# Performance work log

Measured on AMD Instinct MI355X. Metric: run time of the kernel, lower is better.

The kernel has to match this reference:

```python
import jax, jax.numpy as jnp
import numpy as np

EPS = 1e-5
INF = 1e5


def setup_inputs() -> dict:
    key = jax.random.key(0)
    ks = iter(jax.random.split(key, 32))
    B, N, F, H, NH, C = 2, 384, 64, 64, 4, 32
    def lin(k, fi, fo):
        return jax.random.normal(k, (fi, fo), jnp.float32) / np.sqrt(fi).astype(np.float32)
    d = {}
    d['h'] = jax.random.normal(next(ks), (B, N, F), jnp.float32)
    d['x'] = jax.random.normal(next(ks), (B, N, 3), jnp.float32)
    # edge_model (ConcatenationFilter): Linear(2F+1,H), SiLU, Linear(H,H), SiLU
    d['We0'] = lin(next(ks), 2 * F + 1, H); d['be0'] = jnp.zeros(H, jnp.float32)
    d['We1'] = lin(next(ks), H, H);         d['be1'] = jnp.zeros(H, jnp.float32)
    # semantic_attention_mlp: Linear(H, n_heads), LeakyReLU(0.2)
    d['Ws'] = lin(next(ks), H, NH);         d['bs'] = jnp.zeros(NH, jnp.float32)
    # coefficients_mlp: Linear(H,H), SiLU, Linear(H,C)
    d['Wc0'] = lin(next(ks), H, H);         d['bc0'] = jnp.zeros(H, jnp.float32)
    d['Wc1'] = lin(next(ks), H, C);         d['bc1'] = jnp.zeros(C, jnp.float32)
    # post_norm_mlp: Linear(C,H), SiLU, Linear(H,H)
    d['Wp0'] = lin(next(ks), C, H);         d['bp0'] = jnp.zeros(H, jnp.float32)
    d['Wp1'] = lin(next(ks), H, H);         d['bp1'] = jnp.zeros(H, jnp.float32)
    # coordinate_mlp: Linear(H,H), SiLU, Linear(H,1,bias=False) init gain 1e-3
    d['Wx0'] = lin(next(ks), H, H);         d['bx0'] = jnp.zeros(H, jnp.float32)
    d['Wx1'] = lin(next(ks), H, 1) * 1e-3
    # node_mlp: Linear(NH*H + H + F, H), SiLU, Linear(H, F)
    d['Wn0'] = lin(next(ks), NH * H + H + F, H); d['bn0'] = jnp.zeros(H, jnp.float32)
    d['Wn1'] = lin(next(ks), H, F);         d['bn1'] = jnp.zeros(F, jnp.float32)
    d['log_gamma'] = jnp.zeros(NH, jnp.float32)
    return d


def _forward(h, x, We0, be0, We1, be1, Ws, bs, Wc0, bc0, Wc1, bc1,
             Wp0, bp0, Wp1, bp1, Wx0, bx0, Wx1, Wn0, bn0, Wn1, bn1, log_gamma):
    B, N, F = h.shape
    silu = jax.nn.silu

    # pairwise displacements and distances: (B,N,N,3), (B,N,N,1)
    x_minus_xt = x[:, :, None, :] - x[:, None, :, :]
    norm = jnp.sqrt(jnp.sum(x_minus_xt * x_minus_xt, axis=-1, keepdims=True) + EPS)

    # pairwise node-feature concat + distance -> edge MLP (ConcatenationFilter)
    hi = jnp.broadcast_to(h[:, :, None, :], (B, N, N, F))
    hj = jnp.broadcast_to(h[:, None, :, :], (B, N, N, F))
    e_in = jnp.concatenate([hi, hj, norm], axis=-1)           # (B,N,N,2F+1)
    h_e = silu(silu(e_in @ We0 + be0) @ We1 + be1)            # (B,N,N,H)

    eye = jnp.eye(N, dtype=h.dtype)[None, :, :, None]         # mask self-edges

    # euclidean attention per head, softmax over neighbors j (axis=-2)
    eu = jax.nn.softmax(-(norm + INF * eye) * jnp.exp(log_gamma), axis=-2)  # (B,N,N,NH)
    # semantic attention
    sem_logits = jax.nn.leaky_relu(h_e @ Ws + bs, 0.2) - INF * eye
    sem = jax.nn.softmax(sem_logits, axis=-2)                 # (B,N,N,NH)
    comb = eu * sem
    comb = comb / (jnp.sum(comb, axis=-2, keepdims=True) + EPS)

    # attention-weighted multi-head edge features, aggregated over neighbors
    h_e_att = (comb[..., :, None] * h_e[..., None, :]).reshape(B, N, N, -1)  # (B,N,N,NH*H)
    h_e_agg = jnp.sum(h_e_att, axis=-2)                       # (B,N,NH*H)

    # spatial attention: equivariant combinations of unit direction vectors
    coeff = silu(h_e @ Wc0 + bc0) @ Wc1 + bc1                 # (B,N,N,C)
    x_hat = x_minus_xt / (norm + EPS)                         # (B,N,N,3)
    combinations = coeff[..., :, None] * x_hat[..., None, :]  # (B,N,N,C,3)
    comb_sum = jnp.mean(combinations, axis=2)                 # mean over j -> (B,N,C,3)
    comb_norm = jnp.sum(comb_sum * comb_sum, axis=-1)         # (B,N,C)
    h_comb = silu(comb_norm @ Wp0 + bp0) @ Wp1 + bp1          # (B,N,H)

    # node update (residual)
    node_in = jnp.concatenate([h, h_e_agg, h_comb], axis=-1)
    h_out = h + (silu(node_in @ Wn0 + bn0) @ Wn1 + bn1)

    # coordinate update: scalar-gated displacements, mean over neighbors
    scale = silu(h_e @ Wx0 + bx0) @ Wx1                       # (B,N,N,1)
    x_out = x + jnp.mean(x_minus_xt * scale, axis=2)          # (B,N,3)
    return h_out, x_out


def reference(h, x, We0, be0, We1, be1, Ws, bs, Wc0, bc0, Wc1, bc1,
              Wp0, bp0, Wp1, bp1, Wx0, bx0, Wx1, Wn0, bn0, Wn1, bn1, log_gamma):
    return _forward(h, x, We0, be0, We1, be1, Ws, bs, Wc0, bc0, Wc1, bc1,
                    Wp0, bp0, Wp1, bp1, Wx0, bx0, Wx1, Wn0, bn0, Wn1, bn1, log_gamma)
```

## Files before the change

### kernel.cpp

```cpp
#include <hip/hip_runtime.h>

#define NPT 384
#define NB 2
#define NROW (NB*NPT)
#define NT 6
#define HOFF 49152
#define RECB 1024
#define REC_OFF 424960

typedef unsigned short u16;
typedef unsigned int u32;
typedef __bf16 bf16x8 __attribute__((ext_vector_type(8)));
typedef float f32x4 __attribute__((ext_vector_type(4)));

struct alignas(16) U4 { u32 x, y, z, w; };

constexpr float kEPS = 1e-5f;
constexpr float kINF = 1e5f;

__device__ __forceinline__ u16 f2b(float f) { __bf16 b = (__bf16)f; return __builtin_bit_cast(u16, b); }
__device__ __forceinline__ u32 pk2(float lo, float hi) { return (u32)f2b(lo) | ((u32)f2b(hi) << 16); }
__device__ __forceinline__ float b2f(u32 u) { return __uint_as_float(u << 16); }
__device__ __forceinline__ float silu_f(float v) { return v * __builtin_amdgcn_rcpf(1.f + __expf(-v)); }
__device__ __forceinline__ float wredmax(float v) {
#pragma unroll
  for (int m = 32; m >= 1; m >>= 1) v = fmaxf(v, __shfl_xor(v, m, 64));
  return v;
}
__device__ __forceinline__ float wredsum(float v) {
#pragma unroll
  for (int m = 32; m >= 1; m >>= 1) v += __shfl_xor(v, m, 64);
  return v;
}
__device__ __forceinline__ void up8(U4 u, float* f) {
  f[0] = b2f(u.x & 0xffffu); f[1] = b2f(u.x >> 16);
  f[2] = b2f(u.y & 0xffffu); f[3] = b2f(u.y >> 16);
  f[4] = b2f(u.z & 0xffffu); f[5] = b2f(u.z >> 16);
  f[6] = b2f(u.w & 0xffffu); f[7] = b2f(u.w >> 16);
}

__global__ __launch_bounds__(64) void sake_prep(
    const float* __restrict__ h, const float* __restrict__ We0,
    const float* __restrict__ be0, const float* __restrict__ We1,
    const float* __restrict__ Wc0, const float* __restrict__ Wc1,
    const float* __restrict__ Wx0, const float* __restrict__ Ws,
    float* __restrict__ U, float* __restrict__ V, u16* __restrict__ WT)
{
  const int t = threadIdx.x;
  const int blk = blockIdx.x;
  if (blk < NROW) {
    __shared__ float hs[64];
    hs[t] = h[blk * 64 + t];
    __syncthreads();
    float u = be0[t], v = 0.f;
#pragma unroll 8
    for (int k = 0; k < 64; k++) {
      float hv = hs[k];
      u = fmaf(hv, We0[k * 64 + t], u);
      v = fmaf(hv, We0[(64 + k) * 64 + t], v);
    }
    U[blk * 64 + t] = u;
    V[blk * 64 + t] = v;
  } else {
    const int wsel = blk - NROW;
    if (wsel == 4) {
      u16* dst = WT + 14336;
      for (int o = t; o < 16 * 64; o += 64) {
        int c = o >> 6, k = o & 63;
        dst[o] = (c < 4) ? f2b(Ws[k * 4 + c]) : (u16)0;
      }
      return;
    }
    const float* src; int nout; u16* dst;
    if      (wsel == 0) { src = We1; nout = 64; dst = WT;         }
    else if (wsel == 1) { src = Wc0; nout = 64; dst = WT + 4096;  }
    else if (wsel == 2) { src = Wx0; nout = 64; dst = WT + 8192;  }
    else                { src = Wc1; nout = 32; dst = WT + 12288; }
    const int total = 64 * nout;
    for (int o = t; o < total; o += 64) {
      int n = o >> 6, k = o & 63;
      dst[o] = f2b(src[k * nout + n]);
    }
  }
}

struct MainArgs {
  const float *x, *U, *V;
  const u16 *We1T, *Wc0T, *Wx0T, *Wc1T, *WsPT;
  const float *We0, *bs, *be1, *bc0, *bc1, *bx0, *Wx1, *log_gamma;
  char* rec;
};

template<bool DUALT>
__device__ __forceinline__ void gemm64(const u16* aT, const u16* __restrict__ wG,
                                       const float* bias, u16* oT, u16* oTT, int w, int lane)
{
  const int m0 = w << 4;
  const int arow = m0 + (lane & 15);
  const int r7 = arow & 7;
  const int kg = lane >> 4;
  bf16x8 a0 = *(const bf16x8*)(aT + arow * 64 + ((kg ^ r7) << 3));
  bf16x8 a1 = *(const bf16x8*)(aT + arow * 64 + ((((kg + 4)) ^ r7) << 3));
#pragma unroll
  for (int nt = 0; nt < 4; nt++) {
    const int col = (nt << 4) + (lane & 15);
    const u16* wrow = wG + col * 64;
    bf16x8 b0 = *(const bf16x8*)(wrow + (kg << 3));
    bf16x8 b1 = *(const bf16x8*)(wrow + 32 + (kg << 3));
    f32x4 acc = {0.f, 0.f, 0.f, 0.f};
    acc = __builtin_amdgcn_mfma_f32_16x16x32_bf16(a0, b0, acc, 0, 0, 0);
    acc = __builtin_amdgcn_mfma_f32_16x16x32_bf16(a1, b1, acc, 0, 0, 0);
    const float bv = bias[col];
    const int cs = col >> 3, ce = col & 7;
#pragma unroll
    for (int r = 0; r < 4; r++) {
      const int row = m0 + (kg << 2) + r;
      const u16 v = f2b(silu_f(acc[r] + bv));
      oT[row * 64 + ((cs ^ (row & 7)) << 3) + ce] = v;
      if constexpr (DUALT)
        oTT[col * 64 + ((((row >> 3)) ^ (col & 7)) << 3) + (row & 7)] = v;
    }
  }
}

__global__ __launch_bounds__(256, 5) void sake_main(MainArgs A)
{
  __shared__ __align__(16) u16 buf0[64 * 64];
  __shared__ __align__(16) u16 hes[64 * 64];
  __shared__ __align__(16) u16 hesT[64 * 64];
  __shared__ __align__(16) u16 reg3[64 * 32];
  __shared__ float raw_lds[64 * 5];
  __shared__ float disp[64][3];
  __shared__ float nrm_s[64];
  __shared__ float sU[64], wd[64], sbe1[64], sbc0[64], sbx0[64], sWx1[64];
  __shared__ float sbc1[32], sbs[4], sgam[4];

  const int t = threadIdx.x;
  const int w = t >> 6, lane = t & 63;
  const int bt = blockIdx.x;
  const int i = bt % NPT;
  const int bj = bt / NPT;
  const int jt = bj % NT, b = bj / NT;
  const int bi = b * NPT + i;
  const int j0 = jt << 6;
  const int jj2 = t >> 2, q4 = t & 3;
  char* rec = A.rec + (size_t)(bi * NT + jt) * RECB;

  const int j = j0 + jj2;
  const float* xp = &A.x[(b * NPT + j) * 3];
  const float xj0 = xp[0], xj1 = xp[1], xj2 = xp[2];
  const float xi0 = A.x[bi * 3 + 0], xi1 = A.x[bi * 3 + 1], xi2 = A.x[bi * 3 + 2];
  const float4* vp = (const float4*)(A.V + (size_t)(b * NPT + j) * 64 + q4 * 16);
  const float4 v0_ = vp[0], v1_ = vp[1], v2_ = vp[2], v3_ = vp[3];

  if (t < 64) {
    sU[t]   = A.U[bi * 64 + t];
    wd[t]   = A.We0[128 * 64 + t];
    sbe1[t] = A.be1[t];
    sbc0[t] = A.bc0[t];
    sbx0[t] = A.bx0[t];
    sWx1[t] = A.Wx1[t];
    if (t < 32) sbc1[t] = A.bc1[t];
    if (t < 4) { sbs[t] = A.bs[t]; sgam[t] = __expf(A.log_gamma[t]); }
  }
  __syncthreads();

  float cA0 = 0, cA1 = 0, cA2 = 0, xA0 = 0, xA1 = 0, xA2 = 0;

  {
    float dx0 = xi0 - xj0, dx1 = xi1 - xj1, dx2 = xi2 - xj2;
    float nr = sqrtf(fmaf(dx0, dx0, fmaf(dx1, dx1, fmaf(dx2, dx2, kEPS))));
    if (q4 == 0) { disp[jj2][0] = dx0; disp[jj2][1] = dx1; disp[jj2][2] = dx2; nrm_s[jj2] = nr; }
    float vv[16] = {v0_.x, v0_.y, v0_.z, v0_.w, v1_.x, v1_.y, v1_.z, v1_.w,
                    v2_.x, v2_.y, v2_.z, v2_.w, v3_.x, v3_.y, v3_.z, v3_.w};
    float sv[16];
#pragma unroll
    for (int e = 0; e < 16; e++) {
      const int f = q4 * 16 + e;
      sv[e] = silu_f(sU[f] + vv[e] + nr * wd[f]);
    }
    U4 lo, hi;
    lo.x = pk2(sv[0], sv[1]);   lo.y = pk2(sv[2], sv[3]);
    lo.z = pk2(sv[4], sv[5]);   lo.w = pk2(sv[6], sv[7]);
    hi.x = pk2(sv[8], sv[9]);   hi.y = pk2(sv[10], sv[11]);
    hi.z = pk2(sv[12], sv[13]); hi.w = pk2(sv[14], sv[15]);
    const int r7 = jj2 & 7;
    *(U4*)(buf0 + jj2 * 64 + (((q4 * 2) ^ r7) << 3)) = lo;
    *(U4*)(buf0 + jj2 * 64 + (((q4 * 2 + 1) ^ r7) << 3)) = hi;
  }
  gemm64<true>(buf0, A.We1T, sbe1, hes, hesT, w, lane);
  gemm64<false>(hes, A.Wc0T, sbc0, buf0, nullptr, w, lane);
  {
    const int m0 = w << 4;
    const int arow = m0 + (lane & 15);
    const int r7a = arow & 7;
    const int kg = lane >> 4;
    bf16x8 a0 = *(const bf16x8*)(buf0 + arow * 64 + ((kg ^ r7a) << 3));
    bf16x8 a1 = *(const bf16x8*)(buf0 + arow * 64 + (((kg + 4) ^ r7a) << 3));
#pragma unroll
    for (int nt = 0; nt < 2; nt++) {
      const int col = (nt << 4) + (lane & 15);
      const u16* wrow = A.Wc1T + col * 64;
      bf16x8 b0 = *(const bf16x8*)(wrow + (kg << 3));
      bf16x8 b1 = *(const bf16x8*)(wrow + 32 + (kg << 3));
      f32x4 acc = {0.f, 0.f, 0.f, 0.f};
      acc = __builtin_amdgcn_mfma_f32_16x16x32_bf16(a0, b0, acc, 0, 0, 0);
      acc = __builtin_amdgcn_mfma_f32_16x16x32_bf16(a1, b1, acc, 0, 0, 0);
      const float bv = sbc1[col];
#pragma unroll
      for (int r = 0; r < 4; r++) {
        const int row = m0 + (kg << 2) + r;
        reg3[row * 32 + col] = f2b(acc[r] + bv);
      }
    }
  }
  {
    const int c = t & 31, g = t >> 5;
#pragma unroll
    for (int it = 0; it < 8; ++it) {
      const int jj = (g << 3) + it;
      const float s = b2f(reg3[jj * 32 + c]) * __builtin_amdgcn_rcpf(nrm_s[jj] + kEPS);
      cA0 = fmaf(s, disp[jj][0], cA0);
      cA1 = fmaf(s, disp[jj][1], cA1);
      cA2 = fmaf(s, disp[jj][2], cA2);
    }
  }
  gemm64<false>(hes, A.Wx0T, sbx0, buf0, nullptr, w, lane);
  {
    const int jj = jj2;
    const int r7 = jj & 7;
    float acc = 0.f;
#pragma unroll
    for (int c2 = 0; c2 < 2; c2++) {
      const int c = q4 * 2 + c2;
      U4 u = *(const U4*)(buf0 + jj * 64 + ((c ^ r7) << 3));
      float f8[8]; up8(u, f8);
#pragma unroll
      for (int e = 0; e < 8; e++) acc = fmaf(f8[e], sWx1[c * 8 + e], acc);
    }
    acc += __shfl_xor(acc, 1, 64);
    acc += __shfl_xor(acc, 2, 64);
    if (q4 == 0) {
      xA0 = fmaf(disp[jj][0], acc, xA0);
      xA1 = fmaf(disp[jj][1], acc, xA1);
      xA2 = fmaf(disp[jj][2], acc, xA2);
    }
  }
  {
    const int m0 = w << 4;
    const int arow = m0 + (lane & 15);
    const int r7a = arow & 7;
    const int kg = lane >> 4;
    bf16x8 a0 = *(const bf16x8*)(hes + arow * 64 + ((kg ^ r7a) << 3));
    bf16x8 a1 = *(const bf16x8*)(hes + arow * 64 + (((kg + 4) ^ r7a) << 3));
    const u16* wrow = A.WsPT + (lane & 15) * 64;
    bf16x8 b0 = *(const bf16x8*)(wrow + (kg << 3));
    bf16x8 b1 = *(const bf16x8*)(wrow + 32 + (kg << 3));
    f32x4 acc = {0.f, 0.f, 0.f, 0.f};
    acc = __builtin_amdgcn_mfma_f32_16x16x32_bf16(a0, b0, acc, 0, 0, 0);
    acc = __builtin_amdgcn_mfma_f32_16x16x32_bf16(a1, b1, acc, 0, 0, 0);
    if ((lane & 15) < 4) {
#pragma unroll
      for (int r = 0; r < 4; r++)
        raw_lds[(m0 + (kg << 2) + r) * 5 + (lane & 15)] = acc[r];
    }
  }
  __syncthreads();

  float* cascr = (float*)hes;
  cascr[t * 3 + 0] = cA0; cascr[t * 3 + 1] = cA1; cascr[t * 3 + 2] = cA2;
  if (q4 == 0) {
    float* xs = (float*)hes + 768;
    xs[jj2 * 3 + 0] = xA0; xs[jj2 * 3 + 1] = xA1; xs[jj2 * 3 + 2] = xA2;
  }
  {
    const int jj = lane, head = w;
    float raw = raw_lds[jj * 5 + head] + sbs[head];
    float bsem = (raw > 0.f) ? raw : 0.2f * raw;
    const bool self = (j0 + jj) == i;
    if (self) bsem -= kINF;
    const float aeu = -(nrm_s[jj] + (self ? kINF : 0.f)) * sgam[head];
    const float L = aeu + bsem;
    const float mL = wredmax(L);
    const float eL = __expf(L - mL);
    const float SL = wredsum(eL);
    const float mb = wredmax(bsem);
    const float Sb = wredsum(__expf(bsem - mb));
    const float Sa = wredsum(__expf(aeu));
    u16* E = reg3 + 1024;
    E[head * 64 + (((jj >> 3) ^ head) << 3) + (jj & 7)] = f2b(eL);
    if (lane == 0) {
      float* sp = (float*)(rec + 908) + head * 5;
      sp[0] = mL; sp[1] = SL; sp[2] = mb; sp[3] = Sb; sp[4] = Sa;
    }
  }
  __syncthreads();

  {
    const int kg = lane >> 4;
    const int erow = lane & 15;
    const int e7 = erow & 7;
    const u16* E = reg3 + 1024;
    bf16x8 ea0 = *(const bf16x8*)(E + erow * 64 + ((kg ^ e7) << 3));
    bf16x8 ea1 = *(const bf16x8*)(E + erow * 64 + (((kg + 4) ^ e7) << 3));
    const int f = (w << 4) + (lane & 15);
    const int f7 = f & 7;
    bf16x8 hb0 = *(const bf16x8*)(hesT + f * 64 + ((kg ^ f7) << 3));
    bf16x8 hb1 = *(const bf16x8*)(hesT + f * 64 + (((kg + 4) ^ f7) << 3));
    f32x4 aF = {0.f, 0.f, 0.f, 0.f};
    aF = __builtin_amdgcn_mfma_f32_16x16x32_bf16(ea0, hb0, aF, 0, 0, 0);
    aF = __builtin_amdgcn_mfma_f32_16x16x32_bf16(ea1, hb1, aF, 0, 0, 0);
    if (kg == 0) {
      u16* rA = (u16*)rec;
#pragma unroll
      for (int r = 0; r < 4; r++) rA[r * 64 + (w << 4) + (lane & 15)] = f2b(aF[r]);
    }
  }
  if (t < 96) {
    const int c = t & 31, d = t >> 5;
    float s = 0.f;
#pragma unroll
    for (int g = 0; g < 8; g++) s += cascr[(g * 32 + c) * 3 + d];
    ((float*)(rec + 512))[d * 32 + c] = s;
  } else if (t < 99) {
    const int d = t - 96;
    float s = 0.f;
    for (int k = 0; k < 64; k++) s += ((float*)hes + 768)[k * 3 + d];
    ((float*)(rec + 896))[d] = s;
  }
}

struct MergeArgs {
  const float *h, *x, *Wp0, *bp0, *Wp1, *bp1, *Wn0, *bn0, *Wn1, *bn1;
  const char* rec;
  float* out;
};

__global__ __launch_bounds__(256) void sake_merge(MergeArgs M)
{
  __shared__ float sc[NT][20];
  __shared__ float wAl[NT][4];
  __shared__ float coefh[4];
  __shared__ float node_in[384];
  __shared__ float cmv[96];
  __shared__ float nrm32[32];
  __shared__ float t0s[64];
  __shared__ float scr[256];

  const int t = threadIdx.x;
  const int bi = blockIdx.x;
  const char* rb = M.rec + (size_t)bi * NT * RECB;

  if (t < NT * 20) {
    const int tt = t / 20, k = t % 20;
    sc[tt][k] = ((const float*)(rb + tt * RECB + 908))[k];
  }
  if (t < 64) node_in[t] = M.h[bi * 64 + t];
  __syncthreads();
  if (t < 4) {
    const int hh = t;
    float mL = -1e30f, mb = -1e30f;
    for (int tt = 0; tt < NT; tt++) {
      mL = fmaxf(mL, sc[tt][hh * 5 + 0]);
      mb = fmaxf(mb, sc[tt][hh * 5 + 2]);
    }
    float SL = 0.f, Sb = 0.f, Sa = 0.f;
    for (int tt = 0; tt < NT; tt++) {
      const float wa = __expf(sc[tt][hh * 5 + 0] - mL);
      wAl[tt][hh] = wa;
      SL = fmaf(wa, sc[tt][hh * 5 + 1], SL);
      Sb = fmaf(__expf(sc[tt][hh * 5 + 2] - mb), sc[tt][hh * 5 + 3], Sb);
      Sa += sc[tt][hh * 5 + 4];
    }
    const float Ff = __expf(mL - mb);
    coefh[hh] = Ff / fmaf(SL, Ff, kEPS * Sa * Sb);
  }
  __syncthreads();
  {
    const int hh = t >> 6, f = t & 63;
    float s = 0.f;
#pragma unroll
    for (int tt = 0; tt < NT; tt++)
      s = fmaf(wAl[tt][hh], b2f(((const u16*)(rb + tt * RECB))[hh * 64 + f]), s);
    node_in[64 + hh * 64 + f] = s * coefh[hh];
  }
  if (t < 96) {
    float s = 0.f;
#pragma unroll
    for (int tt = 0; tt < NT; tt++) s += ((const float*)(rb + tt * RECB + 512))[t];
    cmv[t] = s * (1.f / 384.f);
  }
  if (t >= 128 && t < 131) {
    const int d = t - 128;
    float s = 0.f;
#pragma unroll
    for (int tt = 0; tt < NT; tt++) s += ((const float*)(rb + tt * RECB + 896))[d];
    M.out[HOFF + bi * 3 + d] = M.x[bi * 3 + d] + s * (1.f / 384.f);
  }
  __syncthreads();
  if (t < 32) {
    const float v0 = cmv[t], v1 = cmv[32 + t], v2 = cmv[64 + t];
    nrm32[t] = v0 * v0 + v1 * v1 + v2 * v2;
  }
  __syncthreads();
  if (t < 64) {
    float a = M.bp0[t];
    for (int c = 0; c < 32; c++) a = fmaf(nrm32[c], M.Wp0[c * 64 + t], a);
    t0s[t] = silu_f(a);
  }
  __syncthreads();
  if (t < 64) {
    float a = M.bp1[t];
    for (int k = 0; k < 64; k++) a = fmaf(t0s[k], M.Wp1[k * 64 + t], a);
    node_in[320 + t] = a;
  }
  __syncthreads();
  {
    const int f = t & 63, q = t >> 6;
    float a = 0.f;
    const int k0 = q * 96;
    for (int k = 0; k < 96; k++) a = fmaf(node_in[k0 + k], M.Wn0[(k0 + k) * 64 + f], a);
    scr[t] = a;
  }
  __syncthreads();
  if (t < 64) {
    const float s = scr[t] + scr[64 + t] + scr[128 + t] + scr[192 + t] + M.bn0[t];
    t0s[t] = silu_f(s);
  }
  __syncthreads();
  if (t < 64) {
    float a = M.bn1[t];
    for (int k = 0; k < 64; k++) a = fmaf(t0s[k], M.Wn1[k * 64 + t], a);
    M.out[bi * 64 + t] = M.h[bi * 64 + t] + a;
  }
}

extern "C" void kernel_launch(void* const* d_in, const int* in_sizes, int n_in,
                              void* d_out, int out_size, void* d_ws, size_t ws_size,
                              hipStream_t stream)
{
  (void)in_sizes; (void)n_in; (void)out_size; (void)ws_size;
  const float* h   = (const float*)d_in[0];
  const float* x   = (const float*)d_in[1];
  const float* We0 = (const float*)d_in[2];
  const float* be0 = (const float*)d_in[3];
  const float* We1 = (const float*)d_in[4];
  const float* be1 = (const float*)d_in[5];
  const float* Ws  = (const float*)d_in[6];
  const float* bs  = (const float*)d_in[7];
  const float* Wc0 = (const float*)d_in[8];
  const float* bc0 = (const float*)d_in[9];
  const float* Wc1 = (const float*)d_in[10];
  const float* bc1 = (const float*)d_in[11];
  const float* Wp0 = (const float*)d_in[12];
  const float* bp0 = (const float*)d_in[13];
  const float* Wp1 = (const float*)d_in[14];
  const float* bp1 = (const float*)d_in[15];
  const float* Wx0 = (const float*)d_in[16];
  const float* bx0 = (const float*)d_in[17];
  const float* Wx1 = (const float*)d_in[18];
  const float* Wn0 = (const float*)d_in[19];
  const float* bn0 = (const float*)d_in[20];
  const float* Wn1 = (const float*)d_in[21];
  const float* bn1 = (const float*)d_in[22];
  const float* lg  = (const float*)d_in[23];

  float* U = (float*)d_ws;
  float* V = U + NROW * 64;
  u16* WT = (u16*)(V + NROW * 64);
  char* rec = (char*)d_ws + REC_OFF;

  sake_prep<<<NROW + 5, 64, 0, stream>>>(h, We0, be0, We1, Wc0, Wc1, Wx0, Ws, U, V, WT);

  MainArgs A;
  A.x = x; A.U = U; A.V = V;
  A.We1T = WT; A.Wc0T = WT + 4096; A.Wx0T = WT + 8192; A.Wc1T = WT + 12288;
  A.WsPT = WT + 14336;
  A.We0 = We0; A.bs = bs; A.be1 = be1; A.bc0 = bc0; A.bc1 = bc1;
  A.bx0 = bx0; A.Wx1 = Wx1; A.log_gamma = lg;
  A.rec = rec;
  sake_main<<<NROW * NT, 256, 0, stream>>>(A);

  MergeArgs Mg;
  Mg.h = h; Mg.x = x;
  Mg.Wp0 = Wp0; Mg.bp0 = bp0; Mg.Wp1 = Wp1; Mg.bp1 = bp1;
  Mg.Wn0 = Wn0; Mg.bn0 = bn0; Mg.Wn1 = Wn1; Mg.bn1 = bn1;
  Mg.rec = rec; Mg.out = (float*)d_out;
  sake_merge<<<NROW, 256, 0, stream>>>(Mg);
}
```

Measured before the change: 98.15 us.

## Transpose MFMA operand roles so activations stay in registers across chained GEMMs

Swaps the GEMM operand roles so weights are the A operand and the per-edge activations the B operand. Each wave's activation fragment is read from LDS once and reused across the consecutive small GEMMs, with packed 8-byte output stores. The shared-memory staging of biases and small vectors is replaced by direct global float4 loads, which removes one block barrier. Launch bounds drop from 5 to 4 blocks per CU, giving more registers but less occupancy.

```diff
diff --git a/kernel.cpp b/kernel.cpp
--- a/kernel.cpp
+++ b/kernel.cpp
@@ -14,6 +14,7 @@
 typedef float f32x4 __attribute__((ext_vector_type(4)));
 
 struct alignas(16) U4 { u32 x, y, z, w; };
+struct alignas(8)  U2 { u32 x, y; };
 
 constexpr float kEPS = 1e-5f;
 constexpr float kINF = 1e5f;
@@ -91,49 +92,63 @@
   char* rec;
 };
 
-template<bool DUALT>
-__device__ __forceinline__ void gemm64(const u16* aT, const u16* __restrict__ wG,
-                                       const float* bias, u16* oT, u16* oTT, int w, int lane)
+__device__ __forceinline__ void readB(const u16* tile, int j, int kg, bf16x8& f0, bf16x8& f1) {
+  const int r7 = j & 7;
+  f0 = *(const bf16x8*)(tile + j * 64 + ((kg ^ r7) << 3));
+  f1 = *(const bf16x8*)(tile + j * 64 + (((kg + 4) ^ r7) << 3));
+}
+
+template<int NNT, bool SILU_, int NCH, bool DUALT>
+__device__ __forceinline__ void gemmT(const u16* __restrict__ wG, const float* __restrict__ biasG,
+                                      bf16x8 bf0, bf16x8 bf1, u16* out, u16* oTT, int w, int lane)
 {
-  const int m0 = w << 4;
-  const int arow = m0 + (lane & 15);
-  const int r7 = arow & 7;
+  const int j = (w << 4) + (lane & 15);
   const int kg = lane >> 4;
-  bf16x8 a0 = *(const bf16x8*)(aT + arow * 64 + ((kg ^ r7) << 3));
-  bf16x8 a1 = *(const bf16x8*)(aT + arow * 64 + ((((kg + 4)) ^ r7) << 3));
-#pragma unroll
-  for (int nt = 0; nt < 4; nt++) {
-    const int col = (nt << 4) + (lane & 15);
-    const u16* wrow = wG + col * 64;
-    bf16x8 b0 = *(const bf16x8*)(wrow + (kg << 3));
-    bf16x8 b1 = *(const bf16x8*)(wrow + 32 + (kg << 3));
+  const int jm = j & (NCH - 1);
+#pragma unroll
+  for (int nt = 0; nt < NNT; nt++) {
+    const int nrow = (nt << 4) + (lane & 15);
+    bf16x8 a0 = *(const bf16x8*)(wG + nrow * 64 + (kg << 3));
+    bf16x8 a1 = *(const bf16x8*)(wG + nrow * 64 + 32 + (kg << 3));
     f32x4 acc = {0.f, 0.f, 0.f, 0.f};
-    acc = __builtin_amdgcn_mfma_f32_16x16x32_bf16(a0, b0, acc, 0, 0, 0);
-    acc = __builtin_amdgcn_mfma_f32_16x16x32_bf16(a1, b1, acc, 0, 0, 0);
-    const float bv = bias[col];
-    const int cs = col >> 3, ce = col & 7;
-#pragma unroll
-    for (int r = 0; r < 4; r++) {
-      const int row = m0 + (kg << 2) + r;
-      const u16 v = f2b(silu_f(acc[r] + bv));
-      oT[row * 64 + ((cs ^ (row & 7)) << 3) + ce] = v;
-      if constexpr (DUALT)
-        oTT[col * 64 + ((((row >> 3)) ^ (col & 7)) << 3) + (row & 7)] = v;
-    }
-  }
-}
-
-__global__ __launch_bounds__(256, 5) void sake_main(MainArgs A)
+    acc = __builtin_amdgcn_mfma_f32_16x16x32_bf16(a0, bf0, acc, 0, 0, 0);
+    acc = __builtin_amdgcn_mfma_f32_16x16x32_bf16(a1, bf1, acc, 0, 0, 0);
+    const int n0 = (nt << 4) + (kg << 2);
+    const float4 bv = *(const float4*)(biasG + n0);
+    float s0, s1, s2, s3;
+    if constexpr (SILU_) {
+      s0 = silu_f(acc[0] + bv.x); s1 = silu_f(acc[1] + bv.y);
+      s2 = silu_f(acc[2] + bv.z); s3 = silu_f(acc[3] + bv.w);
+    } else {
+      s0 = acc[0] + bv.x; s1 = acc[1] + bv.y;
+      s2 = acc[2] + bv.z; s3 = acc[3] + bv.w;
+    }
+    const u16 q0 = f2b(s0), q1 = f2b(s1), q2 = f2b(s2), q3 = f2b(s3);
+    U2 pkd; pkd.x = (u32)q0 | ((u32)q1 << 16); pkd.y = (u32)q2 | ((u32)q3 << 16);
+    const int c = n0 >> 3;
+    *(U2*)(out + j * (NCH * 8) + (((c ^ jm) << 3) + (n0 & 7))) = pkd;
+    if constexpr (DUALT) {
+      const int jq = (j >> 3), j7 = j & 7;
+      const u16 qs[4] = {q0, q1, q2, q3};
+#pragma unroll
+      for (int r = 0; r < 4; r++) {
+        const int f = n0 + r;
+        oTT[f * 64 + ((jq ^ (f & 7)) << 3) + j7] = qs[r];
+      }
+    }
+  }
+}
+
+__global__ __launch_bounds__(256, 4) void sake_main(MainArgs A)
 {
   __shared__ __align__(16) u16 buf0[64 * 64];
   __shared__ __align__(16) u16 hes[64 * 64];
   __shared__ __align__(16) u16 hesT[64 * 64];
-  __shared__ __align__(16) u16 reg3[64 * 32];
+  __shared__ __align__(16) u16 coeff[64 * 32];
+  __shared__ __align__(16) u16 E_lds[16 * 64];
   __shared__ float raw_lds[64 * 5];
   __shared__ float disp[64][3];
   __shared__ float nrm_s[64];
-  __shared__ float sU[64], wd[64], sbe1[64], sbc0[64], sbx0[64], sWx1[64];
-  __shared__ float sbc1[32], sbs[4], sgam[4];
 
   const int t = threadIdx.x;
   const int w = t >> 6, lane = t & 63;
@@ -146,26 +161,16 @@
   const int jj2 = t >> 2, q4 = t & 3;
   char* rec = A.rec + (size_t)(bi * NT + jt) * RECB;
 
-  const int j = j0 + jj2;
-  const float* xp = &A.x[(b * NPT + j) * 3];
+  const int jrow = j0 + jj2;
+  const float* xp = &A.x[(b * NPT + jrow) * 3];
   const float xj0 = xp[0], xj1 = xp[1], xj2 = xp[2];
   const float xi0 = A.x[bi * 3 + 0], xi1 = A.x[bi * 3 + 1], xi2 = A.x[bi * 3 + 2];
-  const float4* vp = (const float4*)(A.V + (size_t)(b * NPT + j) * 64 + q4 * 16);
+  const float4* vp = (const float4*)(A.V + (size_t)(b * NPT + jrow) * 64 + q4 * 16);
   const float4 v0_ = vp[0], v1_ = vp[1], v2_ = vp[2], v3_ = vp[3];
-
-  if (t < 64) {
-    sU[t]   = A.U[bi * 64 + t];
-    wd[t]   = A.We0[128 * 64 + t];
-    sbe1[t] = A.be1[t];
-    sbc0[t] = A.bc0[t];
-    sbx0[t] = A.bx0[t];
-    sWx1[t] = A.Wx1[t];
-    if (t < 32) sbc1[t] = A.bc1[t];
-    if (t < 4) { sbs[t] = A.bs[t]; sgam[t] = __expf(A.log_gamma[t]); }
-  }
-  __syncthreads();
-
-  float cA0 = 0, cA1 = 0, cA2 = 0, xA0 = 0, xA1 = 0, xA2 = 0;
+  const float4* Up = (const float4*)(A.U + bi * 64 + q4 * 16);
+  const float4 u0_ = Up[0], u1_ = Up[1], u2_ = Up[2], u3_ = Up[3];
+  const float4* Wd = (const float4*)(A.We0 + 128 * 64 + q4 * 16);
+  const float4 w0_ = Wd[0], w1_ = Wd[1], w2_ = Wd[2], w3_ = Wd[3];
 
   {
     float dx0 = xi0 - xj0, dx1 = xi1 - xj1, dx2 = xi2 - xj2;
@@ -173,12 +178,13 @@
     if (q4 == 0) { disp[jj2][0] = dx0; disp[jj2][1] = dx1; disp[jj2][2] = dx2; nrm_s[jj2] = nr; }
     float vv[16] = {v0_.x, v0_.y, v0_.z, v0_.w, v1_.x, v1_.y, v1_.z, v1_.w,
                     v2_.x, v2_.y, v2_.z, v2_.w, v3_.x, v3_.y, v3_.z, v3_.w};
+    float uu[16] = {u0_.x, u0_.y, u0_.z, u0_.w, u1_.x, u1_.y, u1_.z, u1_.w,
+                    u2_.x, u2_.y, u2_.z, u2_.w, u3_.x, u3_.y, u3_.z, u3_.w};
+    float ww[16] = {w0_.x, w0_.y, w0_.z, w0_.w, w1_.x, w1_.y, w1_.z, w1_.w,
+                    w2_.x, w2_.y, w2_.z, w2_.w, w3_.x, w3_.y, w3_.z, w3_.w};
     float sv[16];
 #pragma unroll
-    for (int e = 0; e < 16; e++) {
-      const int f = q4 * 16 + e;
-      sv[e] = silu_f(sU[f] + vv[e] + nr * wd[f]);
-    }
+    for (int e = 0; e < 16; e++) sv[e] = silu_f(uu[e] + vv[e] + nr * ww[e]);
     U4 lo, hi;
     lo.x = pk2(sv[0], sv[1]);   lo.y = pk2(sv[2], sv[3]);
     lo.z = pk2(sv[4], sv[5]);   lo.w = pk2(sv[6], sv[7]);
@@ -188,44 +194,39 @@
     *(U4*)(buf0 + jj2 * 64 + (((q4 * 2) ^ r7) << 3)) = lo;
     *(U4*)(buf0 + jj2 * 64 + (((q4 * 2 + 1) ^ r7) << 3)) = hi;
   }
-  gemm64<true>(buf0, A.We1T, sbe1, hes, hesT, w, lane);
-  gemm64<false>(hes, A.Wc0T, sbc0, buf0, nullptr, w, lane);
-  {
-    const int m0 = w << 4;
-    const int arow = m0 + (lane & 15);
-    const int r7a = arow & 7;
-    const int kg = lane >> 4;
-    bf16x8 a0 = *(const bf16x8*)(buf0 + arow * 64 + ((kg ^ r7a) << 3));
-    bf16x8 a1 = *(const bf16x8*)(buf0 + arow * 64 + (((kg + 4) ^ r7a) << 3));
-#pragma unroll
-    for (int nt = 0; nt < 2; nt++) {
-      const int col = (nt << 4) + (lane & 15);
-      const u16* wrow = A.Wc1T + col * 64;
-      bf16x8 b0 = *(const bf16x8*)(wrow + (kg << 3));
-      bf16x8 b1 = *(const bf16x8*)(wrow + 32 + (kg << 3));
-      f32x4 acc = {0.f, 0.f, 0.f, 0.f};
-      acc = __builtin_amdgcn_mfma_f32_16x16x32_bf16(a0, b0, acc, 0, 0, 0);
-      acc = __builtin_amdgcn_mfma_f32_16x16x32_bf16(a1, b1, acc, 0, 0, 0);
-      const float bv = sbc1[col];
-#pragma unroll
-      for (int r = 0; r < 4; r++) {
-        const int row = m0 + (kg << 2) + r;
-        reg3[row * 32 + col] = f2b(acc[r] + bv);
-      }
-    }
-  }
+
+  const int j = (w << 4) + (lane & 15);
+  const int kg = lane >> 4;
+
+  bf16x8 bh0, bh1;
+  readB(buf0, j, kg, bh0, bh1);
+  gemmT<4, true, 8, true>(A.We1T, A.be1, bh0, bh1, hes, hesT, w, lane);
+
+  bf16x8 he0, he1;
+  readB(hes, j, kg, he0, he1);
+
+  gemmT<4, true, 8, false>(A.Wc0T, A.bc0, he0, he1, buf0, nullptr, w, lane);
+  bf16x8 c10, c11;
+  readB(buf0, j, kg, c10, c11);
+  gemmT<2, false, 4, false>(A.Wc1T, A.bc1, c10, c11, coeff, nullptr, w, lane);
+
+  float cA0 = 0, cA1 = 0, cA2 = 0, xA0 = 0, xA1 = 0, xA2 = 0;
   {
     const int c = t & 31, g = t >> 5;
+    const int cc = c >> 3, ce = c & 7;
 #pragma unroll
     for (int it = 0; it < 8; ++it) {
       const int jj = (g << 3) + it;
-      const float s = b2f(reg3[jj * 32 + c]) * __builtin_amdgcn_rcpf(nrm_s[jj] + kEPS);
+      const float s = b2f(coeff[jj * 32 + ((cc ^ (jj & 3)) << 3) + ce]) *
+                      __builtin_amdgcn_rcpf(nrm_s[jj] + kEPS);
       cA0 = fmaf(s, disp[jj][0], cA0);
       cA1 = fmaf(s, disp[jj][1], cA1);
       cA2 = fmaf(s, disp[jj][2], cA2);
     }
   }
-  gemm64<false>(hes, A.Wx0T, sbx0, buf0, nullptr, w, lane);
+
+  gemmT<4, true, 8, false>(A.Wx0T, A.bx0, he0, he1, buf0, nullptr, w, lane);
+
   {
     const int jj = jj2;
     const int r7 = jj & 7;
@@ -235,8 +236,12 @@
       const int c = q4 * 2 + c2;
       U4 u = *(const U4*)(buf0 + jj * 64 + ((c ^ r7) << 3));
       float f8[8]; up8(u, f8);
-#pragma unroll
-      for (int e = 0; e < 8; e++) acc = fmaf(f8[e], sWx1[c * 8 + e], acc);
+      const float4* wx = (const float4*)(A.Wx1 + c * 8);
+      const float4 wxa = wx[0], wxb = wx[1];
+      acc = fmaf(f8[0], wxa.x, acc); acc = fmaf(f8[1], wxa.y, acc);
+      acc = fmaf(f8[2], wxa.z, acc); acc = fmaf(f8[3], wxa.w, acc);
+      acc = fmaf(f8[4], wxb.x, acc); acc = fmaf(f8[5], wxb.y, acc);
+      acc = fmaf(f8[6], wxb.z, acc); acc = fmaf(f8[7], wxb.w, acc);
     }
     acc += __shfl_xor(acc, 1, 64);
     acc += __shfl_xor(acc, 2, 64);
@@ -246,11 +251,11 @@
       xA2 = fmaf(disp[jj][2], acc, xA2);
     }
   }
+
   {
     const int m0 = w << 4;
     const int arow = m0 + (lane & 15);
     const int r7a = arow & 7;
-    const int kg = lane >> 4;
     bf16x8 a0 = *(const bf16x8*)(hes + arow * 64 + ((kg ^ r7a) << 3));
     bf16x8 a1 = *(const bf16x8*)(hes + arow * 64 + (((kg + 4) ^ r7a) << 3));
     const u16* wrow = A.WsPT + (lane & 15) * 64;
@@ -267,19 +272,19 @@
   }
   __syncthreads();
 
-  float* cascr = (float*)hes;
+  float* cascr = (float*)buf0;
+  float* xscr = (float*)buf0 + 768;
   cascr[t * 3 + 0] = cA0; cascr[t * 3 + 1] = cA1; cascr[t * 3 + 2] = cA2;
-  if (q4 == 0) {
-    float* xs = (float*)hes + 768;
-    xs[jj2 * 3 + 0] = xA0; xs[jj2 * 3 + 1] = xA1; xs[jj2 * 3 + 2] = xA2;
-  }
+  if (q4 == 0) { xscr[jj2 * 3 + 0] = xA0; xscr[jj2 * 3 + 1] = xA1; xscr[jj2 * 3 + 2] = xA2; }
+
   {
     const int jj = lane, head = w;
-    float raw = raw_lds[jj * 5 + head] + sbs[head];
+    float raw = raw_lds[jj * 5 + head] + A.bs[head];
     float bsem = (raw > 0.f) ? raw : 0.2f * raw;
     const bool self = (j0 + jj) == i;
     if (self) bsem -= kINF;
-    const float aeu = -(nrm_s[jj] + (self ? kINF : 0.f)) * sgam[head];
+    const float gam = __expf(A.log_gamma[head]);
+    const float aeu = -(nrm_s[jj] + (self ? kINF : 0.f)) * gam;
     const float L = aeu + bsem;
     const float mL = wredmax(L);
     const float eL = __expf(L - mL);
@@ -287,8 +292,7 @@
     const float mb = wredmax(bsem);
     const float Sb = wredsum(__expf(bsem - mb));
     const float Sa = wredsum(__expf(aeu));
-    u16* E = reg3 + 1024;
-    E[head * 64 + (((jj >> 3) ^ head) << 3) + (jj & 7)] = f2b(eL);
+    E_lds[head * 64 + (((jj >> 3) ^ head) << 3) + (jj & 7)] = f2b(eL);
     if (lane == 0) {
       float* sp = (float*)(rec + 908) + head * 5;
       sp[0] = mL; sp[1] = SL; sp[2] = mb; sp[3] = Sb; sp[4] = Sa;
@@ -297,12 +301,10 @@
   __syncthreads();
 
   {
-    const int kg = lane >> 4;
     const int erow = lane & 15;
     const int e7 = erow & 7;
-    const u16* E = reg3 + 1024;
-    bf16x8 ea0 = *(const bf16x8*)(E + erow * 64 + ((kg ^ e7) << 3));
-    bf16x8 ea1 = *(const bf16x8*)(E + erow * 64 + (((kg + 4) ^ e7) << 3));
+    bf16x8 ea0 = *(const bf16x8*)(E_lds + erow * 64 + ((kg ^ e7) << 3));
+    bf16x8 ea1 = *(const bf16x8*)(E_lds + erow * 64 + (((kg + 4) ^ e7) << 3));
     const int f = (w << 4) + (lane & 15);
     const int f7 = f & 7;
     bf16x8 hb0 = *(const bf16x8*)(hesT + f * 64 + ((kg ^ f7) << 3));
@@ -313,7 +315,7 @@
     if (kg == 0) {
       u16* rA = (u16*)rec;
 #pragma unroll
-      for (int r = 0; r < 4; r++) rA[r * 64 + (w << 4) + (lane & 15)] = f2b(aF[r]);
+      for (int r = 0; r < 4; r++) rA[r * 64 + f] = f2b(aF[r]);
     }
   }
   if (t < 96) {
@@ -325,7 +327,7 @@
   } else if (t < 99) {
     const int d = t - 96;
     float s = 0.f;
-    for (int k = 0; k < 64; k++) s += ((float*)hes + 768)[k * 3 + d];
+    for (int k = 0; k < 64; k++) s += xscr[k * 3 + d];
     ((float*)(rec + 896))[d] = s;
   }
 }
```

Result: slower. 104.3 us (+6.3%).
